# Performance work log

Hardware: AMD Instinct MI355X
Metric: run time of the kernel (lower is better)

## Reference

```python
import jax, jax.numpy as jnp
import numpy as np

N_HEAD = 12
D_HEAD = 64


def setup_inputs() -> dict:
    key = jax.random.key(0)
    ks = jax.random.split(key, 9)
    bs, seq, d_model = 4, 2048, 768
    sc = 1.0 / np.sqrt(d_model)
    return {
        "q": jax.random.normal(ks[0], (bs, seq, d_model), jnp.float32),
        "k": jax.random.normal(ks[1], (bs, seq, d_model), jnp.float32),
        "v": jax.random.normal(ks[2], (bs, seq, d_model), jnp.float32),
        "Wq": jax.random.normal(ks[3], (d_model, d_model), jnp.float32) * sc,
        "bq": jax.random.normal(ks[4], (d_model,), jnp.float32) * 0.01,
        "Wk": jax.random.normal(ks[5], (d_model, d_model), jnp.float32) * sc,
        "bk": jax.random.normal(ks[6], (d_model,), jnp.float32) * 0.01,
        "Wv": jax.random.normal(ks[7], (d_model, d_model), jnp.float32) * sc,
        "bv": jax.random.normal(ks[8], (d_model,), jnp.float32) * 0.01,
    }


def _split_heads(x):
    # [bs, seq, n_head*d_head] -> [bs, n_head, seq, d_head]
    bs, seq, _ = x.shape
    return x.reshape(bs, seq, N_HEAD, D_HEAD).transpose(0, 2, 1, 3)


def reference(q, k, v, Wq, bq, Wk, bk, Wv, bv):
    # Linear projections (torch Linear: x @ W.T + b)
    wq = _split_heads(q @ Wq.T + bq)
    wk = _split_heads(k @ Wk.T + bk)
    wv = _split_heads(v @ Wv.T + bv)
    # scale=False in defaults -> raw dot products, no mask, dropout is eval no-op
    scores = jnp.einsum("bhqd,bhkd->bhqk", wq, wk)  # [bs, h, S, S]
    probs = jax.nn.softmax(scores, axis=-1)
    attn_vec = jnp.einsum("bhqk,bhkd->bhqd", probs, wv)
    bs, _, seq, _ = attn_vec.shape
    # merge heads -> [bs, seq, n_head*d_head]
    return attn_vec.transpose(0, 2, 1, 3).reshape(bs, seq, N_HEAD * D_HEAD)
```

## Files before the change

### kernel.cpp

```cpp
#include <hip/hip_runtime.h>
#include <stdint.h>

typedef _Float16 half8  __attribute__((ext_vector_type(8)));
typedef _Float16 half4v __attribute__((ext_vector_type(4)));
typedef float    floatx4 __attribute__((ext_vector_type(4)));

#define LOG2E 1.44269504088896340736f

__device__ __forceinline__ void gl_lds16(const _Float16* g, _Float16* l) {
  __builtin_amdgcn_global_load_lds(
      (__attribute__((address_space(1))) void*)g,
      (__attribute__((address_space(3))) void*)l, 16, 0, 0);
}
__device__ __forceinline__ void gl_lds16f(const float* g, float* l) {
  __builtin_amdgcn_global_load_lds(
      (__attribute__((address_space(1))) void*)g,
      (__attribute__((address_space(3))) void*)l, 16, 0, 0);
}

__device__ __forceinline__ half4v pack4(float a, float b, float c, float d) {
  auto lo = __builtin_amdgcn_cvt_pkrtz(a, b);
  auto hi = __builtin_amdgcn_cvt_pkrtz(c, d);
  return half4v{static_cast<_Float16>(lo[0]), static_cast<_Float16>(lo[1]),
                static_cast<_Float16>(hi[0]), static_cast<_Float16>(hi[1])};
}
__device__ __forceinline__ half8 cvt8(floatx4 a, floatx4 b) {
  half4v lo = pack4(a[0], a[1], a[2], a[3]);
  half4v hi = pack4(b[0], b[1], b[2], b[3]);
  return __builtin_shufflevector(lo, hi, 0, 1, 2, 3, 4, 5, 6, 7);
}

struct CvtArgs {
  const float* src[3];
  _Float16*    dst[3];
};

__global__ void cvt_kernel(CvtArgs a) {
  const int z = blockIdx.y;
  const int i = (blockIdx.x * 256 + threadIdx.x) * 8;
  const float4* s = (const float4*)(a.src[z] + i);
  float4 v0 = s[0], v1 = s[1];
  half8 h = { (_Float16)v0.x, (_Float16)v0.y, (_Float16)v0.z, (_Float16)v0.w,
              (_Float16)v1.x, (_Float16)v1.y, (_Float16)v1.z, (_Float16)v1.w };
  *(half8*)(a.dst[z] + i) = h;
}


__device__ __forceinline__ void gemm_stage(const float* __restrict__ X,
                                           const _Float16* __restrict__ W,
                                           float* Asb, _Float16* Bsb,
                                           int m0, int n0, int k0, int tid) {
  #pragma unroll
  for (int i = 0; i < 4; ++i) {
    int G = i * 256 + tid;
    int r = G >> 3, gl = G & 7;
    int g = gl ^ (r & 7);
    gl_lds16f(X + (size_t)(m0 + r) * 768 + k0 + g * 4, Asb + G * 4);
  }
  #pragma unroll
  for (int i = 0; i < 2; ++i) {
    int G = i * 256 + tid;
    int r = G >> 2, gl = G & 3;
    int g = gl ^ ((r >> 1) & 3);
    gl_lds16(W + (size_t)(n0 + r) * 768 + k0 + g * 8, Bsb + G * 8);
  }
}

template <int BUF>
__device__ __forceinline__ void gemm_body(
    int knext, const float* __restrict__ X, const _Float16* __restrict__ W,
    float* As, _Float16* Bs, int m0, int n0, int tid, int z,
    int wr, int wc, int qd, int col, floatx4 (&acc)[4][4])
{
  if (knext < 768)
    gemm_stage(X, W, As + (1 - BUF) * 4096, Bs + (1 - BUF) * 4096, m0, n0, knext, tid);

  half8 af[4], bf[4];
  #pragma unroll
  for (int t = 0; t < 4; ++t) {
    int ra = wr * 64 + t * 16 + col;
    const float* Ab = As + BUF * 4096 + ra * 32;
    floatx4 a0 = *(const floatx4*)(Ab + (((2 * qd)     ^ (ra & 7)) * 4));
    floatx4 a1 = *(const floatx4*)(Ab + (((2 * qd + 1) ^ (ra & 7)) * 4));
    af[t] = cvt8(a0, a1);
  }
  #pragma unroll
  for (int t = 0; t < 4; ++t) {
    int rb = wc * 64 + t * 16 + col;
    bf[t] = *(const half8*)(Bs + BUF * 4096 + rb * 32 + ((qd ^ ((rb >> 1) & 3)) * 8));
  }
  if (z == 2) {
    #pragma unroll
    for (int i = 0; i < 4; ++i)
      #pragma unroll
      for (int j = 0; j < 4; ++j)
        acc[i][j] = __builtin_amdgcn_mfma_f32_16x16x32_f16(af[i], bf[j], acc[i][j], 0, 0, 0);
  } else {
    #pragma unroll
    for (int i = 0; i < 4; ++i)
      #pragma unroll
      for (int j = 0; j < 4; ++j)
        acc[i][j] = __builtin_amdgcn_mfma_f32_16x16x32_f16(bf[j], af[i], acc[i][j], 0, 0, 0);
  }
  __syncthreads();
}

__global__ __launch_bounds__(256, 2) void qkv_gemm(
    const float* __restrict__ qx, const float* __restrict__ kx, const float* __restrict__ vx,
    const _Float16* __restrict__ wh,
    const float* __restrict__ bqp, const float* __restrict__ bkp, const float* __restrict__ bvp,
    _Float16* __restrict__ oq, _Float16* __restrict__ ok, _Float16* __restrict__ ovt)
{
  __shared__ __attribute__((aligned(16))) char smem[49152];
  float*    As = (float*)smem;
  _Float16* Bs = (_Float16*)(smem + 32768);
  _Float16* Es = (_Float16*)smem;

  const int z  = blockIdx.z;
  const float* X = (z == 0) ? qx : ((z == 1) ? kx : vx);
  const _Float16* W = wh + (size_t)z * 589824;
  const int m0 = blockIdx.x * 128, n0 = blockIdx.y * 128;
  const int tid  = threadIdx.x;
  const int lane = tid & 63, wid = tid >> 6;
  const int wr = wid >> 1, wc = wid & 1;
  const int qd = lane >> 4, col = lane & 15;

  const floatx4 z4 = {0.f, 0.f, 0.f, 0.f};
  floatx4 acc[4][4];
  #pragma unroll
  for (int i = 0; i < 4; ++i)
    #pragma unroll
    for (int j = 0; j < 4; ++j) acc[i][j] = z4;

  gemm_stage(X, W, As, Bs, m0, n0, 0, tid);
  __syncthreads();
  for (int kk = 0; kk < 768; kk += 64) {
    gemm_body<0>(kk + 32, X, W, As, Bs, m0, n0, tid, z, wr, wc, qd, col, acc);
    gemm_body<1>(kk + 64, X, W, As, Bs, m0, n0, tid, z, wr, wc, qd, col, acc);
  }

  const float* bias = (z == 0) ? bqp : ((z == 1) ? bkp : bvp);
  const int b = m0 >> 11, s0 = m0 & 2047;
  if (z == 2) {
    #pragma unroll
    for (int j = 0; j < 4; ++j) {
      int n_loc = wc * 64 + j * 16 + col;
      float bb = bias[n0 + n_loc];
      #pragma unroll
      for (int i = 0; i < 4; ++i) {
        int s_loc = wr * 64 + i * 16 + qd * 4;
        half4v h = pack4(acc[i][j][0] + bb, acc[i][j][1] + bb,
                         acc[i][j][2] + bb, acc[i][j][3] + bb);
        *(half4v*)(Es + n_loc * 160 + s_loc) = h;
      }
    }
    __syncthreads();
    #pragma unroll
    for (int it = 0; it < 8; ++it) {
      int row = it * 16 + (tid >> 4);
      int k   = tid & 15;
      half8 vr = *(const half8*)(Es + row * 160 + k * 8);
      *(half8*)(ovt + ((size_t)(b * 768 + n0 + row)) * 2048 + s0 + k * 8) = vr;
    }
  } else {
    _Float16* O = (z == 0) ? oq : ok;
    const float scale = (z == 0) ? LOG2E : 1.0f;
    #pragma unroll
    for (int j = 0; j < 4; ++j) {
      int n_loc = wc * 64 + j * 16 + qd * 4;
      float4 bb = *(const float4*)(bias + n0 + n_loc);
      #pragma unroll
      for (int i = 0; i < 4; ++i) {
        int s_loc = wr * 64 + i * 16 + col;
        half4v h = pack4((acc[i][j][0] + bb.x) * scale, (acc[i][j][1] + bb.y) * scale,
                         (acc[i][j][2] + bb.z) * scale, (acc[i][j][3] + bb.w) * scale);
        *(half4v*)(Es + s_loc * 160 + n_loc) = h;
      }
    }
    __syncthreads();
    const int hh0 = n0 >> 6;
    #pragma unroll
    for (int it = 0; it < 8; ++it) {
      int seg = it * 32 + (tid >> 3);
      int s = seg >> 1, hseg = seg & 1;
      int k = tid & 7;
      half8 vr = *(const half8*)(Es + s * 160 + hseg * 64 + k * 8);
      int mb = (m0 + s) >> 11, sg = (m0 + s) & 2047;
      *(half8*)(O + (size_t)(mb * 12 + hh0 + hseg) * 131072
                  + (size_t)sg * 64 + k * 8) = vr;
    }
  }
}


__device__ __forceinline__ void stage_kv(const _Float16* __restrict__ Kg,
                                         const _Float16* __restrict__ Vg,
                                         _Float16* ksd, _Float16* vsd, int j0, int tid) {
  #pragma unroll
  for (int i = 0; i < 2; ++i) {
    int c = i * 256 + tid;
    int row = c >> 3, sc = c & 7;
    gl_lds16(Kg + (size_t)(j0 + row) * 64 + ((sc ^ (row & 7)) * 8), ksd + c * 8);
    gl_lds16(Vg + (size_t)row * 2048 + j0 + ((sc ^ (row & 7)) * 8), vsd + c * 8);
  }
}

template <int BUF>
__device__ __forceinline__ void attn_body(
    int jnext, const _Float16* __restrict__ Kg, const _Float16* __restrict__ Vg,
    _Float16* Ks, _Float16* Vs, int tid,
    const half8 (&qf)[2][2], int kb0, int kb1, const int (&vb)[4],
    floatx4 (&negm)[2], floatx4 (&ol)[2], floatx4 (&o)[4][2])
{
  if (jnext < 2048)
    stage_kv(Kg, Vg, Ks + (1 - BUF) * 4096, Vs + (1 - BUF) * 4096, jnext, tid);

  const char* ksb = (const char*)Ks;
  const char* vsb = (const char*)Vs;

  floatx4 st[4][2];
  #pragma unroll
  for (int t = 0; t < 4; ++t) {
    half8 kf0 = *(const half8*)(ksb + BUF * 8192 + t * 2048 + kb0);
    half8 kf1 = *(const half8*)(ksb + BUF * 8192 + t * 2048 + kb1);
    #pragma unroll
    for (int qt = 0; qt < 2; ++qt) {
      st[t][qt] = __builtin_amdgcn_mfma_f32_16x16x32_f16(kf0, qf[qt][0], negm[qt], 0, 0, 0);
      st[t][qt] = __builtin_amdgcn_mfma_f32_16x16x32_f16(kf1, qf[qt][1], st[t][qt], 0, 0, 0);
    }
  }

  float mr[2];
  #pragma unroll
  for (int qt = 0; qt < 2; ++qt) {
    float v = fmaxf(
        fmaxf(fmaxf(fmaxf(st[0][qt][0], st[0][qt][1]), fmaxf(st[0][qt][2], st[0][qt][3])),
              fmaxf(fmaxf(st[1][qt][0], st[1][qt][1]), fmaxf(st[1][qt][2], st[1][qt][3]))),
        fmaxf(fmaxf(fmaxf(st[2][qt][0], st[2][qt][1]), fmaxf(st[2][qt][2], st[2][qt][3])),
              fmaxf(fmaxf(st[3][qt][0], st[3][qt][1]), fmaxf(st[3][qt][2], st[3][qt][3]))));
    v = fmaxf(v, __shfl_xor(v, 16, 64));
    v = fmaxf(v, __shfl_xor(v, 32, 64));
    mr[qt] = fmaxf(v, 0.f);
  }

  half4v pf[4][2];
  #pragma unroll
  for (int qt = 0; qt < 2; ++qt)
    #pragma unroll
    for (int t = 0; t < 4; ++t)
      pf[t][qt] = pack4(__builtin_amdgcn_exp2f(st[t][qt][0] - mr[qt]),
                        __builtin_amdgcn_exp2f(st[t][qt][1] - mr[qt]),
                        __builtin_amdgcn_exp2f(st[t][qt][2] - mr[qt]),
                        __builtin_amdgcn_exp2f(st[t][qt][3] - mr[qt]));

  if (__any(mr[0] > 0.f || mr[1] > 0.f)) {
    #pragma unroll
    for (int qt = 0; qt < 2; ++qt) {
      float al = __builtin_amdgcn_exp2f(-mr[qt]);
      negm[qt] -= mr[qt];
      ol[qt] *= al;
      #pragma unroll
      for (int dt = 0; dt < 4; ++dt) o[dt][qt] *= al;
    }
  }

  const half4v vone = {(_Float16)1.0f, (_Float16)1.0f, (_Float16)1.0f, (_Float16)1.0f};
  #pragma unroll
  for (int dt = 0; dt < 4; ++dt) {
    #pragma unroll
    for (int t = 0; t < 4; ++t) {
      half4v vf = *(const half4v*)(vsb + BUF * 8192 + dt * 2048 + vb[t]);
      #pragma unroll
      for (int qt = 0; qt < 2; ++qt)
        o[dt][qt] = __builtin_amdgcn_mfma_f32_16x16x16f16(vf, pf[t][qt], o[dt][qt], 0, 0, 0);
    }
  }
  #pragma unroll
  for (int t = 0; t < 4; ++t)
    #pragma unroll
    for (int qt = 0; qt < 2; ++qt)
      ol[qt] = __builtin_amdgcn_mfma_f32_16x16x16f16(vone, pf[t][qt], ol[qt], 0, 0, 0);

  __syncthreads();
}

__global__ __launch_bounds__(256, 3) void attn_kernel(
    const _Float16* __restrict__ Qm,
    const _Float16* __restrict__ Km,
    const _Float16* __restrict__ Vt,
    float* __restrict__ out)
{
  __shared__ __attribute__((aligned(16))) _Float16 Ks[2 * 4096];
  __shared__ __attribute__((aligned(16))) _Float16 Vs[2 * 4096];
  const int bh = blockIdx.x;
  const int q0 = blockIdx.y * 128;
  const int tid = threadIdx.x, lane = tid & 63, w = tid >> 6;
  const int qd = lane >> 4, col = lane & 15, c7 = col & 7;
  const _Float16* Qg = Qm + (size_t)bh * 131072;
  const _Float16* Kg = Km + (size_t)bh * 131072;
  const _Float16* Vg = Vt + (size_t)bh * 131072;

  half8 qf[2][2];
  #pragma unroll
  for (int qt = 0; qt < 2; ++qt)
    #pragma unroll
    for (int ks = 0; ks < 2; ++ks)
      qf[qt][ks] = *(const half8*)(Qg + (size_t)(q0 + w * 32 + qt * 16 + col) * 64
                                   + (ks * 4 + qd) * 8);

  const int kb0 = col * 128 + ((qd ^ c7) * 16);
  const int kb1 = col * 128 + (((4 + qd) ^ c7) * 16);
  const int vq = (qd >> 1) ^ c7;
  int vb[4];
  #pragma unroll
  for (int t = 0; t < 4; ++t)
    vb[t] = col * 128 + (qd & 1) * 8 + ((vq ^ (2 * t)) * 16);

  floatx4 negm[2] = {{100.f, 100.f, 100.f, 100.f}, {100.f, 100.f, 100.f, 100.f}};
  const floatx4 z4 = {0.f, 0.f, 0.f, 0.f};
  floatx4 ol[2] = {z4, z4};
  floatx4 o[4][2];
  #pragma unroll
  for (int dt = 0; dt < 4; ++dt)
    #pragma unroll
    for (int qt = 0; qt < 2; ++qt) o[dt][qt] = z4;

  stage_kv(Kg, Vg, Ks, Vs, 0, tid);
  __syncthreads();

  for (int jj = 0; jj < 2048; jj += 128) {
    attn_body<0>(jj + 64,  Kg, Vg, Ks, Vs, tid, qf, kb0, kb1, vb, negm, ol, o);
    attn_body<1>(jj + 128, Kg, Vg, Ks, Vs, tid, qf, kb0, kb1, vb, negm, ol, o);
  }

  const int b = bh / 12, h = bh % 12;
  #pragma unroll
  for (int qt = 0; qt < 2; ++qt) {
    float inv = 1.0f / ol[qt][0];
    int qg = q0 + w * 32 + qt * 16 + col;
    float* obase = out + ((size_t)b * 2048 + qg) * 768 + h * 64;
    #pragma unroll
    for (int dt = 0; dt < 4; ++dt) {
      floatx4 v = o[dt][qt];
      v *= inv;
      *(floatx4*)(obase + dt * 16 + qd * 4) = v;
    }
  }
}

extern "C" void kernel_launch(void* const* d_in, const int* in_sizes, int n_in,
                              void* d_out, int out_size, void* d_ws, size_t ws_size,
                              hipStream_t stream) {
  const float* q  = (const float*)d_in[0];
  const float* k  = (const float*)d_in[1];
  const float* v  = (const float*)d_in[2];
  const float* Wq = (const float*)d_in[3];
  const float* bq = (const float*)d_in[4];
  const float* Wk = (const float*)d_in[5];
  const float* bk = (const float*)d_in[6];
  const float* Wv = (const float*)d_in[7];
  const float* bv = (const float*)d_in[8];

  const size_t NX = 6291456;
  const size_t NW = 589824;
  const size_t need = (3 * NW + 3 * NX) * sizeof(_Float16);
  if (ws_size < need) return;

  _Float16* wh = (_Float16*)d_ws;
  _Float16* qh = wh + 3 * NW;
  _Float16* kh = qh + NX;
  _Float16* vt = kh + NX;

  CvtArgs ca;
  ca.src[0] = Wq; ca.src[1] = Wk; ca.src[2] = Wv;
  ca.dst[0] = wh; ca.dst[1] = wh + NW; ca.dst[2] = wh + 2 * NW;

  cvt_kernel<<<dim3(288, 3), 256, 0, stream>>>(ca);
  qkv_gemm<<<dim3(64, 6, 3), 256, 0, stream>>>(q, k, v, wh, bq, bk, bv, qh, kh, vt);
  attn_kernel<<<dim3(48, 16), 256, 0, stream>>>(qh, kh, vt, (float*)d_out);
}
```

Baseline: 254.2 us.

## Use 2-wave attention blocks with 64 queries per wave and register-staged V prefetch

The attention kernel drops from 4 waves to 2 waves per 128-query block, so each wave handles 64 query rows (4 q-tiles). Each K/V fragment read from LDS is then reused across twice as many MFMAs, and there are fewer barriers per unit of work. V is now prefetched through registers: it is loaded from global before the softmax and written to LDS with a new XOR swizzle afterwards, while K still uses direct global-to-LDS loads with precomputed pointers. The online-softmax rescale now branches per q-tile, skipping the max subtraction when no row max grows. The trade-off is heavier register pressure (launch bounds 128,2) and fewer waves per CU for latency hiding.

Result: slower. 346.3 us (+36.2%).

```diff
diff --git a/kernel.cpp b/kernel.cpp
--- a/kernel.cpp
+++ b/kernel.cpp
@@ -44,7 +44,6 @@
               (_Float16)v1.x, (_Float16)v1.y, (_Float16)v1.z, (_Float16)v1.w };
   *(half8*)(a.dst[z] + i) = h;
 }
-
 
 __device__ __forceinline__ void gemm_stage(const float* __restrict__ X,
                                            const _Float16* __restrict__ W,
@@ -193,74 +192,84 @@
 }
 
 
-__device__ __forceinline__ void stage_kv(const _Float16* __restrict__ Kg,
-                                         const _Float16* __restrict__ Vg,
-                                         _Float16* ksd, _Float16* vsd, int j0, int tid) {
-  #pragma unroll
-  for (int i = 0; i < 2; ++i) {
-    int c = i * 256 + tid;
-    int row = c >> 3, sc = c & 7;
-    gl_lds16(Kg + (size_t)(j0 + row) * 64 + ((sc ^ (row & 7)) * 8), ksd + c * 8);
-    gl_lds16(Vg + (size_t)row * 2048 + j0 + ((sc ^ (row & 7)) * 8), vsd + c * 8);
-  }
-}
-
 template <int BUF>
 __device__ __forceinline__ void attn_body(
-    int jnext, const _Float16* __restrict__ Kg, const _Float16* __restrict__ Vg,
-    _Float16* Ks, _Float16* Vs, int tid,
-    const half8 (&qf)[2][2], int kb0, int kb1, const int (&vb)[4],
-    floatx4 (&negm)[2], floatx4 (&ol)[2], floatx4 (&o)[4][2])
+    bool pref, const _Float16*& kp, const _Float16*& vp,
+    _Float16* Ks, char* Vs, int tid, int vwA, int vwB,
+    const half8 (&qf)[4][2], int kb0, int kb1, const int (&vb)[4],
+    float (&nm)[4], floatx4 (&ol)[4], floatx4 (&o)[4][4])
 {
-  if (jnext < 2048)
-    stage_kv(Kg, Vg, Ks + (1 - BUF) * 4096, Vs + (1 - BUF) * 4096, jnext, tid);
-
-  const char* ksb = (const char*)Ks;
-  const char* vsb = (const char*)Vs;
-
-  floatx4 st[4][2];
+  int4 vr[4];
+  if (pref) {
+    _Float16* ksd = Ks + (1 - BUF) * 4096;
+    #pragma unroll
+    for (int i = 0; i < 4; ++i)
+      gl_lds16(kp + i * 1024, ksd + (i * 128 + tid) * 8);
+    #pragma unroll
+    for (int i = 0; i < 4; ++i)
+      vr[i] = *(const int4*)(vp + (size_t)i * 32768);
+    kp += 4096;
+    vp += 64;
+  }
+
+  const char* ksb = (const char*)Ks + BUF * 8192;
+  const char* vsb = Vs + BUF * 8192;
+
+  half8 kf0[4], kf1[4];
   #pragma unroll
   for (int t = 0; t < 4; ++t) {
-    half8 kf0 = *(const half8*)(ksb + BUF * 8192 + t * 2048 + kb0);
-    half8 kf1 = *(const half8*)(ksb + BUF * 8192 + t * 2048 + kb1);
-    #pragma unroll
-    for (int qt = 0; qt < 2; ++qt) {
-      st[t][qt] = __builtin_amdgcn_mfma_f32_16x16x32_f16(kf0, qf[qt][0], negm[qt], 0, 0, 0);
-      st[t][qt] = __builtin_amdgcn_mfma_f32_16x16x32_f16(kf1, qf[qt][1], st[t][qt], 0, 0, 0);
-    }
-  }
-
-  float mr[2];
-  #pragma unroll
-  for (int qt = 0; qt < 2; ++qt) {
+    kf0[t] = *(const half8*)(ksb + t * 2048 + kb0);
+    kf1[t] = *(const half8*)(ksb + t * 2048 + kb1);
+  }
+
+  half4v pf[4][4];
+  #pragma unroll
+  for (int qt = 0; qt < 4; ++qt) {
+    floatx4 seed = {nm[qt], nm[qt], nm[qt], nm[qt]};
+    floatx4 st[4];
+    #pragma unroll
+    for (int t = 0; t < 4; ++t) {
+      st[t] = __builtin_amdgcn_mfma_f32_16x16x32_f16(kf0[t], qf[qt][0], seed, 0, 0, 0);
+      st[t] = __builtin_amdgcn_mfma_f32_16x16x32_f16(kf1[t], qf[qt][1], st[t], 0, 0, 0);
+    }
     float v = fmaxf(
-        fmaxf(fmaxf(fmaxf(st[0][qt][0], st[0][qt][1]), fmaxf(st[0][qt][2], st[0][qt][3])),
-              fmaxf(fmaxf(st[1][qt][0], st[1][qt][1]), fmaxf(st[1][qt][2], st[1][qt][3]))),
-        fmaxf(fmaxf(fmaxf(st[2][qt][0], st[2][qt][1]), fmaxf(st[2][qt][2], st[2][qt][3])),
-              fmaxf(fmaxf(st[3][qt][0], st[3][qt][1]), fmaxf(st[3][qt][2], st[3][qt][3]))));
+        fmaxf(fmaxf(fmaxf(st[0][0], st[0][1]), fmaxf(st[0][2], st[0][3])),
+              fmaxf(fmaxf(st[1][0], st[1][1]), fmaxf(st[1][2], st[1][3]))),
+        fmaxf(fmaxf(fmaxf(st[2][0], st[2][1]), fmaxf(st[2][2], st[2][3])),
+              fmaxf(fmaxf(st[3][0], st[3][1]), fmaxf(st[3][2], st[3][3]))));
     v = fmaxf(v, __shfl_xor(v, 16, 64));
     v = fmaxf(v, __shfl_xor(v, 32, 64));
-    mr[qt] = fmaxf(v, 0.f);
-  }
-
-  half4v pf[4][2];
-  #pragma unroll
-  for (int qt = 0; qt < 2; ++qt)
-    #pragma unroll
-    for (int t = 0; t < 4; ++t)
-      pf[t][qt] = pack4(__builtin_amdgcn_exp2f(st[t][qt][0] - mr[qt]),
-                        __builtin_amdgcn_exp2f(st[t][qt][1] - mr[qt]),
-                        __builtin_amdgcn_exp2f(st[t][qt][2] - mr[qt]),
-                        __builtin_amdgcn_exp2f(st[t][qt][3] - mr[qt]));
-
-  if (__any(mr[0] > 0.f || mr[1] > 0.f)) {
-    #pragma unroll
-    for (int qt = 0; qt < 2; ++qt) {
-      float al = __builtin_amdgcn_exp2f(-mr[qt]);
-      negm[qt] -= mr[qt];
+    if (__any(v > 0.f)) {
+      float mr = fmaxf(v, 0.f);
+      float al = __builtin_amdgcn_exp2f(-mr);
+      nm[qt] -= mr;
       ol[qt] *= al;
       #pragma unroll
       for (int dt = 0; dt < 4; ++dt) o[dt][qt] *= al;
+      #pragma unroll
+      for (int t = 0; t < 4; ++t)
+        pf[t][qt] = pack4(__builtin_amdgcn_exp2f(st[t][0] - mr),
+                          __builtin_amdgcn_exp2f(st[t][1] - mr),
+                          __builtin_amdgcn_exp2f(st[t][2] - mr),
+                          __builtin_amdgcn_exp2f(st[t][3] - mr));
+    } else {
+      #pragma unroll
+      for (int t = 0; t < 4; ++t)
+        pf[t][qt] = pack4(__builtin_amdgcn_exp2f(st[t][0]),
+                          __builtin_amdgcn_exp2f(st[t][1]),
+                          __builtin_amdgcn_exp2f(st[t][2]),
+                          __builtin_amdgcn_exp2f(st[t][3]));
+    }
+  }
+
+  if (pref) {
+    char* vsd = Vs + (1 - BUF) * 8192;
+    #pragma unroll
+    for (int i = 0; i < 4; ++i) {
+      int2 lo; lo.x = vr[i].x; lo.y = vr[i].y;
+      int2 hi; hi.x = vr[i].z; hi.y = vr[i].w;
+      *(int2*)(vsd + vwA + i * 2048) = lo;
+      *(int2*)(vsd + vwB + i * 2048) = hi;
     }
   }
 
@@ -269,29 +278,29 @@
   for (int dt = 0; dt < 4; ++dt) {
     #pragma unroll
     for (int t = 0; t < 4; ++t) {
-      half4v vf = *(const half4v*)(vsb + BUF * 8192 + dt * 2048 + vb[t]);
-      #pragma unroll
-      for (int qt = 0; qt < 2; ++qt)
+      half4v vf = *(const half4v*)(vsb + dt * 2048 + vb[t]);
+      #pragma unroll
+      for (int qt = 0; qt < 4; ++qt)
         o[dt][qt] = __builtin_amdgcn_mfma_f32_16x16x16f16(vf, pf[t][qt], o[dt][qt], 0, 0, 0);
     }
   }
   #pragma unroll
   for (int t = 0; t < 4; ++t)
     #pragma unroll
-    for (int qt = 0; qt < 2; ++qt)
+    for (int qt = 0; qt < 4; ++qt)
       ol[qt] = __builtin_amdgcn_mfma_f32_16x16x16f16(vone, pf[t][qt], ol[qt], 0, 0, 0);
 
   __syncthreads();
 }
 
-__global__ __launch_bounds__(256, 3) void attn_kernel(
+__global__ __launch_bounds__(128, 2) void attn_kernel(
     const _Float16* __restrict__ Qm,
     const _Float16* __restrict__ Km,
     const _Float16* __restrict__ Vt,
     float* __restrict__ out)
 {
   __shared__ __attribute__((aligned(16))) _Float16 Ks[2 * 4096];
-  __shared__ __attribute__((aligned(16))) _Float16 Vs[2 * 4096];
+  __shared__ __attribute__((aligned(16))) char     Vs[2 * 8192];
   const int bh = blockIdx.x;
   const int q0 = blockIdx.y * 128;
   const int tid = threadIdx.x, lane = tid & 63, w = tid >> 6;
@@ -300,44 +309,67 @@
   const _Float16* Kg = Km + (size_t)bh * 131072;
   const _Float16* Vg = Vt + (size_t)bh * 131072;
 
-  half8 qf[2][2];
-  #pragma unroll
-  for (int qt = 0; qt < 2; ++qt)
+  half8 qf[4][2];
+  #pragma unroll
+  for (int qt = 0; qt < 4; ++qt)
     #pragma unroll
     for (int ks = 0; ks < 2; ++ks)
-      qf[qt][ks] = *(const half8*)(Qg + (size_t)(q0 + w * 32 + qt * 16 + col) * 64
+      qf[qt][ks] = *(const half8*)(Qg + (size_t)(q0 + w * 64 + qt * 16 + col) * 64
                                    + (ks * 4 + qd) * 8);
 
   const int kb0 = col * 128 + ((qd ^ c7) * 16);
   const int kb1 = col * 128 + (((4 + qd) ^ c7) * 16);
-  const int vq = (qd >> 1) ^ c7;
+  const int rsz = ((col >> 3) ^ col) & 1;
   int vb[4];
   #pragma unroll
   for (int t = 0; t < 4; ++t)
-    vb[t] = col * 128 + (qd & 1) * 8 + ((vq ^ (2 * t)) * 16);
-
-  floatx4 negm[2] = {{100.f, 100.f, 100.f, 100.f}, {100.f, 100.f, 100.f, 100.f}};
+    vb[t] = col * 128 + ((((2 * t) | (qd >> 1)) ^ c7) * 16) + (((qd & 1) ^ rsz) * 8);
+
+  const int r0 = tid >> 3, scg = tid & 7;
+  const int gsw = scg ^ (r0 & 7);
+  const int wsz = ((r0 >> 3) ^ r0) & 1;
+  const int vwA = r0 * 128 + gsw * 16 + wsz * 8;
+  const int vwB = r0 * 128 + gsw * 16 + (wsz ^ 1) * 8;
+  const _Float16* kp = Kg + r0 * 64 + gsw * 8;
+  const _Float16* vp = Vg + (size_t)r0 * 2048 + scg * 8;
+
+  float nm[4] = {100.f, 100.f, 100.f, 100.f};
   const floatx4 z4 = {0.f, 0.f, 0.f, 0.f};
-  floatx4 ol[2] = {z4, z4};
-  floatx4 o[4][2];
+  floatx4 ol[4] = {z4, z4, z4, z4};
+  floatx4 o[4][4];
   #pragma unroll
   for (int dt = 0; dt < 4; ++dt)
     #pragma unroll
-    for (int qt = 0; qt < 2; ++qt) o[dt][qt] = z4;
-
-  stage_kv(Kg, Vg, Ks, Vs, 0, tid);
+    for (int qt = 0; qt < 4; ++qt) o[dt][qt] = z4;
+
+  {
+    #pragma unroll
+    for (int i = 0; i < 4; ++i)
+      gl_lds16(kp + i * 1024, Ks + (i * 128 + tid) * 8);
+    int4 v0[4];
+    #pragma unroll
+    for (int i = 0; i < 4; ++i) v0[i] = *(const int4*)(vp + (size_t)i * 32768);
+    kp += 4096; vp += 64;
+    #pragma unroll
+    for (int i = 0; i < 4; ++i) {
+      int2 lo; lo.x = v0[i].x; lo.y = v0[i].y;
+      int2 hi; hi.x = v0[i].z; hi.y = v0[i].w;
+      *(int2*)(Vs + vwA + i * 2048) = lo;
+      *(int2*)(Vs + vwB + i * 2048) = hi;
+    }
+  }
   __syncthreads();
 
   for (int jj = 0; jj < 2048; jj += 128) {
-    attn_body<0>(jj + 64,  Kg, Vg, Ks, Vs, tid, qf, kb0, kb1, vb, negm, ol, o);
-    attn_body<1>(jj + 128, Kg, Vg, Ks, Vs, tid, qf, kb0, kb1, vb, negm, ol, o);
+    attn_body<0>(true,              kp, vp, Ks, Vs, tid, vwA, vwB, qf, kb0, kb1, vb, nm, ol, o);
+    attn_body<1>(jj + 128 < 2048,   kp, vp, Ks, Vs, tid, vwA, vwB, qf, kb0, kb1, vb, nm, ol, o);
   }
 
   const int b = bh / 12, h = bh % 12;
   #pragma unroll
-  for (int qt = 0; qt < 2; ++qt) {
+  for (int qt = 0; qt < 4; ++qt) {
     float inv = 1.0f / ol[qt][0];
-    int qg = q0 + w * 32 + qt * 16 + col;
+    int qg = q0 + w * 64 + qt * 16 + col;
     float* obase = out + ((size_t)b * 2048 + qg) * 768 + h * 64;
     #pragma unroll
     for (int dt = 0; dt < 4; ++dt) {
@@ -377,5 +409,5 @@
 
   cvt_kernel<<<dim3(288, 3), 256, 0, stream>>>(ca);
   qkv_gemm<<<dim3(64, 6, 3), 256, 0, stream>>>(q, k, v, wh, bq, bk, bv, qh, kh, vt);
-  attn_kernel<<<dim3(48, 16), 256, 0, stream>>>(qh, kh, vt, (float*)d_out);
-}
+  attn_kernel<<<dim3(48, 16), 128, 0, stream>>>(qh, kh, vt, (float*)d_out);
+}
```

## Stage fp32 activations through registers and store fp16 tiles in LDS

Applied to the files above, without the earlier changes.

The QKV projection GEMM previously copied fp32 activation tiles straight into LDS with global_load_lds and converted them to fp16 on every fragment read. It now loads the fp32 activations into registers during the prefetch, converts them once to fp16, and writes them to LDS after the MFMA block. The A tile then uses the same swizzled fp16 layout as B. This halves LDS usage for A, shrinks shared memory from 48KB to 40KB, and allows launch_bounds to request 3 blocks per CU. The cost is extra register pressure from holding the prefetched data, and the A load no longer goes directly from global memory to LDS.

After: 391.6 us. 54.0% more time.

```diff
diff --git a/kernel.cpp b/kernel.cpp
--- a/kernel.cpp
+++ b/kernel.cpp
@@ -8,11 +8,6 @@
 #define LOG2E 1.44269504088896340736f
 
 __device__ __forceinline__ void gl_lds16(const _Float16* g, _Float16* l) {
-  __builtin_amdgcn_global_load_lds(
-      (__attribute__((address_space(1))) void*)g,
-      (__attribute__((address_space(3))) void*)l, 16, 0, 0);
-}
-__device__ __forceinline__ void gl_lds16f(const float* g, float* l) {
   __builtin_amdgcn_global_load_lds(
       (__attribute__((address_space(1))) void*)g,
       (__attribute__((address_space(3))) void*)l, 16, 0, 0);
@@ -23,11 +18,6 @@
   auto hi = __builtin_amdgcn_cvt_pkrtz(c, d);
   return half4v{static_cast<_Float16>(lo[0]), static_cast<_Float16>(lo[1]),
                 static_cast<_Float16>(hi[0]), static_cast<_Float16>(hi[1])};
-}
-__device__ __forceinline__ half8 cvt8(floatx4 a, floatx4 b) {
-  half4v lo = pack4(a[0], a[1], a[2], a[3]);
-  half4v hi = pack4(b[0], b[1], b[2], b[3]);
-  return __builtin_shufflevector(lo, hi, 0, 1, 2, 3, 4, 5, 6, 7);
 }
 
 struct CvtArgs {
@@ -46,17 +36,35 @@
 }
 
 
-__device__ __forceinline__ void gemm_stage(const float* __restrict__ X,
-                                           const _Float16* __restrict__ W,
-                                           float* Asb, _Float16* Bsb,
-                                           int m0, int n0, int k0, int tid) {
-  #pragma unroll
-  for (int i = 0; i < 4; ++i) {
+__device__ __forceinline__ void gemm_issueA(const float* __restrict__ X,
+                                            int m0, int k0, int tid,
+                                            float4 (&ar)[2][2]) {
+  #pragma unroll
+  for (int i = 0; i < 2; ++i) {
     int G = i * 256 + tid;
-    int r = G >> 3, gl = G & 7;
-    int g = gl ^ (r & 7);
-    gl_lds16f(X + (size_t)(m0 + r) * 768 + k0 + g * 4, Asb + G * 4);
-  }
+    int r = G >> 2, gl = G & 3;
+    int g = gl ^ ((r >> 1) & 3);
+    const float4* s = (const float4*)(X + (size_t)(m0 + r) * 768 + k0 + g * 8);
+    ar[i][0] = s[0];
+    ar[i][1] = s[1];
+  }
+}
+
+__device__ __forceinline__ void gemm_writeA(_Float16* Asb, int tid,
+                                            const float4 (&ar)[2][2]) {
+  #pragma unroll
+  for (int i = 0; i < 2; ++i) {
+    int G = i * 256 + tid;
+    half8 h = { (_Float16)ar[i][0].x, (_Float16)ar[i][0].y,
+                (_Float16)ar[i][0].z, (_Float16)ar[i][0].w,
+                (_Float16)ar[i][1].x, (_Float16)ar[i][1].y,
+                (_Float16)ar[i][1].z, (_Float16)ar[i][1].w };
+    *(half8*)(Asb + G * 8) = h;
+  }
+}
+
+__device__ __forceinline__ void gemm_stageB(const _Float16* __restrict__ W,
+                                            _Float16* Bsb, int n0, int k0, int tid) {
   #pragma unroll
   for (int i = 0; i < 2; ++i) {
     int G = i * 256 + tid;
@@ -69,20 +77,21 @@
 template <int BUF>
 __device__ __forceinline__ void gemm_body(
     int knext, const float* __restrict__ X, const _Float16* __restrict__ W,
-    float* As, _Float16* Bs, int m0, int n0, int tid, int z,
+    _Float16* As, _Float16* Bs, int m0, int n0, int tid, int z,
     int wr, int wc, int qd, int col, floatx4 (&acc)[4][4])
 {
-  if (knext < 768)
-    gemm_stage(X, W, As + (1 - BUF) * 4096, Bs + (1 - BUF) * 4096, m0, n0, knext, tid);
+  const bool pref = (knext < 768);
+  float4 ar[2][2];
+  if (pref) {
+    gemm_issueA(X, m0, knext, tid, ar);
+    gemm_stageB(W, Bs + (1 - BUF) * 4096, n0, knext, tid);
+  }
 
   half8 af[4], bf[4];
   #pragma unroll
   for (int t = 0; t < 4; ++t) {
     int ra = wr * 64 + t * 16 + col;
-    const float* Ab = As + BUF * 4096 + ra * 32;
-    floatx4 a0 = *(const floatx4*)(Ab + (((2 * qd)     ^ (ra & 7)) * 4));
-    floatx4 a1 = *(const floatx4*)(Ab + (((2 * qd + 1) ^ (ra & 7)) * 4));
-    af[t] = cvt8(a0, a1);
+    af[t] = *(const half8*)(As + BUF * 4096 + ra * 32 + ((qd ^ ((ra >> 1) & 3)) * 8));
   }
   #pragma unroll
   for (int t = 0; t < 4; ++t) {
@@ -102,18 +111,21 @@
       for (int j = 0; j < 4; ++j)
         acc[i][j] = __builtin_amdgcn_mfma_f32_16x16x32_f16(bf[j], af[i], acc[i][j], 0, 0, 0);
   }
+
+  if (pref)
+    gemm_writeA(As + (1 - BUF) * 4096, tid, ar);
   __syncthreads();
 }
 
-__global__ __launch_bounds__(256, 2) void qkv_gemm(
+__global__ __launch_bounds__(256, 3) void qkv_gemm(
     const float* __restrict__ qx, const float* __restrict__ kx, const float* __restrict__ vx,
     const _Float16* __restrict__ wh,
     const float* __restrict__ bqp, const float* __restrict__ bkp, const float* __restrict__ bvp,
     _Float16* __restrict__ oq, _Float16* __restrict__ ok, _Float16* __restrict__ ovt)
 {
-  __shared__ __attribute__((aligned(16))) char smem[49152];
-  float*    As = (float*)smem;
-  _Float16* Bs = (_Float16*)(smem + 32768);
+  __shared__ __attribute__((aligned(16))) char smem[40960];
+  _Float16* As = (_Float16*)smem;
+  _Float16* Bs = (_Float16*)(smem + 16384);
   _Float16* Es = (_Float16*)smem;
 
   const int z  = blockIdx.z;
@@ -132,7 +144,12 @@
     #pragma unroll
     for (int j = 0; j < 4; ++j) acc[i][j] = z4;
 
-  gemm_stage(X, W, As, Bs, m0, n0, 0, tid);
+  {
+    float4 ar[2][2];
+    gemm_issueA(X, m0, 0, tid, ar);
+    gemm_stageB(W, Bs, n0, 0, tid);
+    gemm_writeA(As, tid, ar);
+  }
   __syncthreads();
   for (int kk = 0; kk < 768; kk += 64) {
     gemm_body<0>(kk + 32, X, W, As, Bs, m0, n0, tid, z, wr, wc, qd, col, acc);
```
